# Kernel tuning notes

Measured on AMD Instinct MI355X. Metric: run time of the kernel, lower is better.

## Reference

```python
import jax, jax.numpy as jnp
import numpy as np

B, L, D_MODEL = 2, 2048, 1024
HEADS, DH, K = 8, 128, 64  # d_head = d_model // heads, kernel_width window
DILATIONS = np.array([1, 1, 2, 2, 4, 4, 8, 8], dtype=np.int32)  # per-head dilation


def setup_inputs() -> dict:
    key = jax.random.key(0)
    ks = jax.random.split(key, 8)
    s_in = 1.0 / np.sqrt(D_MODEL)       # kaiming-uniform-ish fan_in bound
    s_c = 1.0 / np.sqrt(HEADS * DH)
    return {
        "query": jax.random.normal(ks[0], (B, L, D_MODEL), dtype=jnp.float32),
        "key": jax.random.normal(ks[1], (B, L, D_MODEL), dtype=jnp.float32),
        "value": jax.random.normal(ks[2], (B, L, D_MODEL), dtype=jnp.float32),
        "Wq": jax.random.uniform(ks[3], (HEADS, DH, D_MODEL), minval=-s_in, maxval=s_in),
        "bq": jnp.zeros((HEADS, DH), dtype=jnp.float32),
        "Wk": jax.random.uniform(ks[4], (HEADS, DH, D_MODEL), minval=-s_in, maxval=s_in),
        "bk": jnp.zeros((HEADS, DH), dtype=jnp.float32),
        "Wv": jax.random.uniform(ks[5], (HEADS, DH, D_MODEL), minval=-s_in, maxval=s_in),
        "bv": jnp.zeros((HEADS, DH), dtype=jnp.float32),
        "Wc": jax.random.uniform(ks[6], (D_MODEL, HEADS * DH), minval=-s_c, maxval=s_c),
        "bc": jnp.zeros((D_MODEL,), dtype=jnp.float32),
    }


def reference(query, key, value, Wq, bq, Wk, bk, Wv, bv, Wc, bc):
    Lq = query.shape[-2]
    # per-head linear projections: [B,L,D] x [H,DH,D] -> [B,H,L,DH]
    q = jnp.einsum('bld,hed->bhle', query, Wq) + bq[:, None, :]
    k = jnp.einsum('bld,hed->bhle', key, Wk) + bk[:, None, :]
    v = jnp.einsum('bld,hed->bhle', value, Wv) + bv[:, None, :]

    # dilated, centered local windows (per-head dilation)
    offsets = jnp.arange(K) - (K - 1) // 2                     # [K]
    dil = jnp.asarray(DILATIONS)                               # [H]
    idx = (jnp.arange(Lq)[None, :, None]
           + offsets[None, None, :] * dil[:, None, None])      # [H, L, K]
    valid = (idx >= 0) & (idx < Lq)
    idxc = jnp.clip(idx, 0, Lq - 1)

    # gather per-head windows: x [B,H,L,DH], idx [H,L,K] -> [B,H,L,K,DH]
    gather = jax.vmap(lambda xh, ih: xh[:, ih], in_axes=(1, 0), out_axes=1)
    k_win = gather(k, idxc)
    v_win = gather(v, idxc)

    # banded attention (original applies no 1/sqrt(d) scaling)
    scores = jnp.einsum('bhld,bhlkd->bhlk', q, k_win)
    scores = jnp.where(valid[None], scores, jnp.asarray(-1e9, scores.dtype))
    attn = jax.nn.softmax(scores, axis=-1)
    out = jnp.einsum('bhlk,bhlkd->bhld', attn, v_win)

    # merge heads and collapse back to d_model
    out = out.transpose(0, 2, 1, 3).reshape(out.shape[0], Lq, HEADS * DH)
    return out @ Wc.T + bc
```

## Files before the change

### kernel.cpp

```cpp
#include <hip/hip_runtime.h>
#include <hip/hip_bf16.h>
#include <stdint.h>

#define NB 2
#define LQ 2048
#define DMODEL 1024
#define NH 8
#define DH 128
#define KWIN 64

typedef __attribute__((ext_vector_type(8))) short short8;
typedef __attribute__((ext_vector_type(4))) float f32x4;

__device__ __forceinline__ ushort f2bf(float f) {
  uint u = __float_as_uint(f);
  return (ushort)((u + 0x7fffu + ((u >> 16) & 1u)) >> 16);
}
__device__ __forceinline__ float bflo(uint u) { return __uint_as_float(u << 16); }
__device__ __forceinline__ float bfhi(uint u) { return __uint_as_float(u & 0xffff0000u); }

__global__ void cvt_all(const float4* __restrict__ q, const float4* __restrict__ k,
                        const float4* __restrict__ v, const float4* __restrict__ wq,
                        const float4* __restrict__ wk, const float4* __restrict__ wv,
                        const float4* __restrict__ wc, ushort4* __restrict__ dst) {
  const int n4in = (NB * LQ * DMODEL) / 4;
  const int n4w = (NH * DH * DMODEL) / 4;
  const int total = 3 * n4in + 4 * n4w;
  const int stride = gridDim.x * blockDim.x;
  for (int i = blockIdx.x * blockDim.x + threadIdx.x; i < total; i += stride) {
    const float4* src;
    int off;
    if (i < 3 * n4in) {
      const int r = i >> 20;
      off = i & (n4in - 1);
      src = (r == 0) ? q : ((r == 1) ? k : v);
    } else {
      const int j = i - 3 * n4in;
      const int r = j >> 18;
      off = j & (n4w - 1);
      src = (r == 0) ? wq : ((r == 1) ? wk : ((r == 2) ? wv : wc));
    }
    float4 x = src[off];
    dst[i] = make_ushort4(f2bf(x.x), f2bf(x.y), f2bf(x.z), f2bf(x.w));
  }
}

__global__ __launch_bounds__(512, 2) void gemm256_qkv(
    const ushort* __restrict__ A0, const ushort* __restrict__ B0,
    const float* __restrict__ c0, ushort* __restrict__ D0,
    const ushort* __restrict__ A1, const ushort* __restrict__ B1,
    const float* __restrict__ c1, ushort* __restrict__ D1,
    const ushort* __restrict__ A2, const ushort* __restrict__ B2,
    const float* __restrict__ c2, ushort* __restrict__ D2,
    int M, int N, int Kd) {
  const int gx = gridDim.x, gy = gridDim.y;
  const int nblk = gx * gy * gridDim.z;
  const int fid = (blockIdx.z * gy + blockIdx.y) * gx + blockIdx.x;
  const int cpx = nblk >> 3;
  const int nid = (fid & 7) * cpx + (fid >> 3);
  const int z = nid / (gx * gy);
  const int rem = nid % (gx * gy);
  const int m0 = (rem / gx) * 256;
  const int n0 = (rem % gx) * 256;

  const ushort* A = (z == 0) ? A0 : ((z == 1) ? A1 : A2);
  const ushort* Bt = (z == 0) ? B0 : ((z == 1) ? B1 : B2);
  const float* bias = (z == 0) ? c0 : ((z == 1) ? c1 : c2);
  ushort* Cv = (z == 0) ? D0 : ((z == 1) ? D1 : D2);

  __shared__ ushort LDS[4 * 16384];

  const int tid = threadIdx.x;
  const int wave = tid >> 6, lane = tid & 63;
  const int wm = wave >> 2, wn = wave & 3;
  const int lrow = lane & 15, kgrp = lane >> 4;

  const int b = tid * 16;
  const int srow = b >> 6;
  const int scc = (b & 63) >> 1;

  const ushort* gA0 = A + (size_t)(m0 + srow) * Kd + scc;
  const ushort* gA1 = A + (size_t)(m0 + 128 + srow) * Kd + scc;
  const ushort* gB0 = Bt + (size_t)(n0 + srow) * Kd + scc;
  const ushort* gB1 = Bt + (size_t)(n0 + 128 + srow) * Kd + scc;
  const int dso = b >> 1;

  auto STAGE = [&](int slot, int kt) {
    ushort* sl = LDS + slot * 16384;
    __builtin_amdgcn_global_load_lds(
        (const __attribute__((address_space(1))) void*)(gA0 + kt),
        (__attribute__((address_space(3))) void*)(sl + dso), 16, 0, 0);
    __builtin_amdgcn_global_load_lds(
        (const __attribute__((address_space(1))) void*)(gA1 + kt),
        (__attribute__((address_space(3))) void*)(sl + 4096 + dso), 16, 0, 0);
    __builtin_amdgcn_global_load_lds(
        (const __attribute__((address_space(1))) void*)(gB0 + kt),
        (__attribute__((address_space(3))) void*)(sl + 8192 + dso), 16, 0, 0);
    __builtin_amdgcn_global_load_lds(
        (const __attribute__((address_space(1))) void*)(gB1 + kt),
        (__attribute__((address_space(3))) void*)(sl + 12288 + dso), 16, 0, 0);
  };

  f32x4 acc[8][4] = {};
  const int NT = Kd >> 5;

  STAGE(0, 0);
  STAGE(1, 32);
  STAGE(2, 64);

  for (int t = 0; t < NT; ++t) {
    const int pf = t + 3;
    if (pf < NT) {
      STAGE(pf & 3, pf << 5);
      asm volatile("s_waitcnt vmcnt(12)" ::: "memory");
    } else if (pf == NT) {
      asm volatile("s_waitcnt vmcnt(8)" ::: "memory");
    } else if (pf == NT + 1) {
      asm volatile("s_waitcnt vmcnt(4)" ::: "memory");
    } else {
      asm volatile("s_waitcnt vmcnt(0)" ::: "memory");
    }
    __builtin_amdgcn_s_barrier();
    __builtin_amdgcn_sched_barrier(0);

    const ushort* sA = LDS + (t & 3) * 16384 + wm * 4096 + lrow * 32 + kgrp * 8;
    const ushort* sB = LDS + (t & 3) * 16384 + 8192 + (wn >> 1) * 4096 +
                       ((wn & 1) * 64 + lrow) * 32 + kgrp * 8;
    short8 af[8], bfr[4];
#pragma unroll
    for (int m = 0; m < 8; ++m) af[m] = *(const short8*)(sA + m * 512);
#pragma unroll
    for (int n = 0; n < 4; ++n) bfr[n] = *(const short8*)(sB + n * 512);
    asm volatile("s_waitcnt lgkmcnt(0)" ::: "memory");
    __builtin_amdgcn_sched_barrier(0);
    __builtin_amdgcn_s_barrier();

#pragma unroll
    for (int m = 0; m < 8; ++m)
#pragma unroll
      for (int n = 0; n < 4; ++n)
        acc[m][n] = __builtin_amdgcn_mfma_f32_16x16x32_bf16(af[m], bfr[n], acc[m][n], 0, 0, 0);
  }

  const int cbase = n0 + wn * 64;
  const int rbase = m0 + wm * 128;
  float bv[4];
#pragma unroll
  for (int n = 0; n < 4; ++n) bv[n] = bias[cbase + n * 16 + lrow];

#pragma unroll
  for (int m = 0; m < 8; ++m) {
#pragma unroll
    for (int n = 0; n < 4; ++n) {
      const int col = cbase + n * 16 + lrow;
#pragma unroll
      for (int j = 0; j < 4; ++j) {
        const int row = rbase + m * 16 + kgrp * 4 + j;
        Cv[(size_t)row * N + col] = f2bf(acc[m][n][j] + bv[n]);
      }
    }
  }
}

__global__ __launch_bounds__(256, 4) void gemm_out(
    const ushort* __restrict__ A, const ushort* __restrict__ Bt,
    const float* __restrict__ bias, float* __restrict__ Cv, int M, int N, int Kd) {
  const int gx = gridDim.x, gy = gridDim.y;
  const int nblk = gx * gy;
  const int fid = blockIdx.y * gx + blockIdx.x;
  const int cpx = nblk >> 3;
  const int nid = (fid & 7) * cpx + (fid >> 3);
  const int m0 = (nid / gx) * 128;
  const int n0 = (nid % gx) * 128;

  __shared__ ushort As[2][128 * 32];
  __shared__ ushort Bs[2][128 * 32];

  const int tid = threadIdx.x;
  const int wave = tid >> 6, lane = tid & 63;
  const int wm = wave >> 1, wn = wave & 1;
  const int lrow = lane & 15, kgrp = lane >> 4;

  const int b0 = tid * 16;
  const int b1 = b0 + 4096;
  const int r0 = b0 >> 6, cc0 = (b0 & 63) >> 1;
  const int r1 = b1 >> 6, cc1 = (b1 & 63) >> 1;

  const ushort* gA0 = A + (size_t)(m0 + r0) * Kd + cc0;
  const ushort* gA1 = A + (size_t)(m0 + r1) * Kd + cc1;
  const ushort* gB0 = Bt + (size_t)(n0 + r0) * Kd + cc0;
  const ushort* gB1 = Bt + (size_t)(n0 + r1) * Kd + cc1;

  auto stage = [&](int buf, int kt) {
    __builtin_amdgcn_global_load_lds(
        (const __attribute__((address_space(1))) void*)(gA0 + kt),
        (__attribute__((address_space(3))) void*)(As[buf] + (b0 >> 1)), 16, 0, 0);
    __builtin_amdgcn_global_load_lds(
        (const __attribute__((address_space(1))) void*)(gA1 + kt),
        (__attribute__((address_space(3))) void*)(As[buf] + (b1 >> 1)), 16, 0, 0);
    __builtin_amdgcn_global_load_lds(
        (const __attribute__((address_space(1))) void*)(gB0 + kt),
        (__attribute__((address_space(3))) void*)(Bs[buf] + (b0 >> 1)), 16, 0, 0);
    __builtin_amdgcn_global_load_lds(
        (const __attribute__((address_space(1))) void*)(gB1 + kt),
        (__attribute__((address_space(3))) void*)(Bs[buf] + (b1 >> 1)), 16, 0, 0);
  };

  f32x4 acc[4][4] = {};

  auto compute = [&](int buf) {
    short8 af[4], bfr[4];
#pragma unroll
    for (int m = 0; m < 4; ++m)
      af[m] = *(const short8*)(As[buf] + (wm * 64 + m * 16 + lrow) * 32 + kgrp * 8);
#pragma unroll
    for (int n = 0; n < 4; ++n)
      bfr[n] = *(const short8*)(Bs[buf] + (wn * 64 + n * 16 + lrow) * 32 + kgrp * 8);
#pragma unroll
    for (int m = 0; m < 4; ++m)
#pragma unroll
      for (int n = 0; n < 4; ++n)
        acc[m][n] = __builtin_amdgcn_mfma_f32_16x16x32_bf16(af[m], bfr[n], acc[m][n], 0, 0, 0);
  };

  const int nt = Kd >> 5;
  stage(0, 0);
  __syncthreads();
  int cur = 0;
  for (int it = 0; it < nt - 1; ++it) {
    stage(cur ^ 1, (it + 1) << 5);
    compute(cur);
    __syncthreads();
    cur ^= 1;
  }
  compute(cur);

  const int cbase = n0 + wn * 64;
  const int rbase = m0 + wm * 64;
  float bv[4];
#pragma unroll
  for (int n = 0; n < 4; ++n) bv[n] = bias[cbase + n * 16 + lrow];

#pragma unroll
  for (int m = 0; m < 4; ++m) {
#pragma unroll
    for (int n = 0; n < 4; ++n) {
      const int col = cbase + n * 16 + lrow;
#pragma unroll
      for (int j = 0; j < 4; ++j) {
        const int row = rbase + m * 16 + kgrp * 4 + j;
        Cv[(size_t)row * N + col] = acc[m][n][j] + bv[n];
      }
    }
  }
}

__global__ __launch_bounds__(128) void banded_attn_mfma(
    const ushort* __restrict__ qp, const ushort* __restrict__ kp,
    const ushort* __restrict__ vp, ushort* __restrict__ ao) {
  __shared__ ushort Qs[32 * 128];
  __shared__ ushort Ks[96 * 128];
  __shared__ ushort Vs[112 * 128];
  __shared__ ushort Ps[2][16 * 104];
  __shared__ ushort Os[2][16 * 128];

  const int tid = threadIdx.x;
  const int wv = tid >> 6;
  const int lane = tid & 63;
  const int lrow = lane & 15, kgrp = lane >> 4;

  const int blk = blockIdx.x;
  const int chunk = blk & 63;
  const int h = (blk >> 6) & 7;
  const int b = blk >> 9;
  const int sh = h >> 1;
  const int dil = 1 << sh;
  const int Ld = LQ >> sh;
  const int rres = chunk >> (6 - sh);
  const int tile = chunk & ((64 >> sh) - 1);
  const int t0 = tile << 5;
  const int p0 = t0 - 32;

  const size_t headoff = (size_t)h * DH;
  const size_t bbase = (size_t)b * LQ * (NH * DH);

  const int srow = lane >> 4;
  const int sc = lane & 15;
  for (int it = wv; it < 60; it += 2) {
    int rbase, pstart;
    const ushort* g;
    ushort* ld;
    if (it < 8) {
      rbase = it * 4; pstart = t0; g = qp; ld = Qs;
    } else if (it < 32) {
      rbase = (it - 8) * 4; pstart = p0; g = kp; ld = Ks;
    } else {
      rbase = (it - 32) * 4; pstart = p0; g = vp; ld = Vs;
    }
    int row = rbase + srow;
    int key = (row ^ (row >> 3)) & 7;
    int cs = sc ^ key;
    int t = pstart + row;
    t = t < 0 ? 0 : (t >= Ld ? Ld - 1 : t);
    int l = rres + t * dil;
    const ushort* src = g + bbase + (size_t)l * (NH * DH) + headoff + cs * 8;
    __builtin_amdgcn_global_load_lds(
        (const __attribute__((address_space(1))) void*)src,
        (__attribute__((address_space(3))) void*)(ld + rbase * 128), 16, 0, 0);
  }
  __syncthreads();

  const int iblk = wv << 4;
  f32x4 accs[5] = {};
#pragma unroll
  for (int ks = 0; ks < 4; ++ks) {
    const int qrow = iblk + lrow;
    const int qslot = (ks * 4 + kgrp) ^ ((qrow ^ (qrow >> 3)) & 7);
    short8 qf = *(const short8*)(Qs + qrow * 128 + qslot * 8);
#pragma unroll
    for (int t = 0; t < 5; ++t) {
      const int krow = (wv + t) * 16 + lrow;
      const int kslot = (ks * 4 + kgrp) ^ ((krow ^ (krow >> 3)) & 7);
      short8 kf = *(const short8*)(Ks + krow * 128 + kslot * 8);
      accs[t] = __builtin_amdgcn_mfma_f32_16x16x32_bf16(qf, kf, accs[t], 0, 0, 0);
    }
  }

  float dens[4];
#pragma unroll
  for (int j = 0; j < 4; ++j) {
    const int i_b = iblk + kgrp * 4 + j;
    float mj = -1e30f;
#pragma unroll
    for (int t = 0; t < 5; ++t) {
      const int jj = (wv + t) * 16 + lrow;
      const int p = p0 + jj;
      const bool ok = (jj >= i_b + 1) && (jj <= i_b + 64) && (p >= 0) && (p < Ld);
      float v = ok ? accs[t][j] : -1e30f;
      accs[t][j] = v;
      mj = fmaxf(mj, v);
    }
#pragma unroll
    for (int off = 1; off < 16; off <<= 1) mj = fmaxf(mj, __shfl_xor(mj, off));
    float dj = 0.f;
#pragma unroll
    for (int t = 0; t < 5; ++t) {
      float e = __expf(accs[t][j] - mj);
      accs[t][j] = e;
      dj += e;
    }
#pragma unroll
    for (int off = 1; off < 16; off <<= 1) dj += __shfl_xor(dj, off);
    dens[j] = dj;
  }

  ushort* Pw = Ps[wv];
#pragma unroll
  for (int j = 0; j < 4; ++j) {
    const int prow = kgrp * 4 + j;
#pragma unroll
    for (int t = 0; t < 5; ++t) Pw[prow * 104 + t * 16 + lrow] = f2bf(accs[t][j]);
    Pw[prow * 104 + 80 + lrow] = 0;
  }

  f32x4 accv[8] = {};
#pragma unroll
  for (int ks = 0; ks < 3; ++ks) {
    short8 pf = *(const short8*)(Pw + lrow * 104 + ks * 32 + kgrp * 8);
#pragma unroll
    for (int dt = 0; dt < 8; ++dt) {
      short8 vf;
#pragma unroll
      for (int rr = 0; rr < 8; ++rr) {
        const int vrow = iblk + ks * 32 + kgrp * 8 + rr;
        const int d = dt * 16 + lrow;
        const int slot = (d >> 3) ^ ((vrow ^ (vrow >> 3)) & 7);
        vf[rr] = (short)Vs[vrow * 128 + slot * 8 + (d & 7)];
      }
      accv[dt] = __builtin_amdgcn_mfma_f32_16x16x32_bf16(pf, vf, accv[dt], 0, 0, 0);
    }
  }

  ushort* Ow = Os[wv];
#pragma unroll
  for (int j = 0; j < 4; ++j) {
    const float inv = 1.f / dens[j];
    const int orow = kgrp * 4 + j;
#pragma unroll
    for (int dt = 0; dt < 8; ++dt)
      Ow[orow * 128 + dt * 16 + lrow] = f2bf(accv[dt][j] * inv);
  }
#pragma unroll
  for (int pass = 0; pass < 4; ++pass) {
    const int i_loc = pass * 4 + srow;
    const int tq = t0 + iblk + i_loc;
    const int l = rres + tq * dil;
    short8 vvv = *(const short8*)(Ow + i_loc * 128 + sc * 8);
    *(short8*)(ao + bbase + (size_t)l * (NH * DH) + headoff + sc * 8) = vvv;
  }
}

extern "C" void kernel_launch(void* const* d_in, const int* in_sizes, int n_in,
                              void* d_out, int out_size, void* d_ws, size_t ws_size,
                              hipStream_t stream) {
  const float* q = (const float*)d_in[0];
  const float* k = (const float*)d_in[1];
  const float* v = (const float*)d_in[2];
  const float* Wq = (const float*)d_in[3];
  const float* bq = (const float*)d_in[4];
  const float* Wk = (const float*)d_in[5];
  const float* bk = (const float*)d_in[6];
  const float* Wv = (const float*)d_in[7];
  const float* bv = (const float*)d_in[8];
  const float* Wc = (const float*)d_in[9];
  const float* bc = (const float*)d_in[10];

  const size_t NIN = (size_t)NB * LQ * DMODEL;
  const size_t NW = (size_t)NH * DH * DMODEL;

  ushort* qin = (ushort*)d_ws;
  ushort* kin = qin + NIN;
  ushort* vin = kin + NIN;
  ushort* wqb = vin + NIN;
  ushort* wkb = wqb + NW;
  ushort* wvb = wkb + NW;
  ushort* wcb = wvb + NW;
  ushort* qp = wcb + NW;
  ushort* kp = qp + NIN;
  ushort* vp = kp + NIN;
  ushort* aob = vp + NIN;

  hipLaunchKernelGGL(cvt_all, dim3(2048), dim3(256), 0, stream,
                     (const float4*)q, (const float4*)k, (const float4*)v,
                     (const float4*)Wq, (const float4*)Wk, (const float4*)Wv,
                     (const float4*)Wc, (ushort4*)qin);

  dim3 g1(DMODEL / 256, (NB * LQ) / 256, 3);
  hipLaunchKernelGGL(gemm256_qkv, g1, dim3(512), 0, stream,
                     qin, wqb, bq, qp,
                     kin, wkb, bk, kp,
                     vin, wvb, bv, vp,
                     NB * LQ, DMODEL, DMODEL);

  hipLaunchKernelGGL(banded_attn_mfma, dim3(NB * NH * 64), dim3(128), 0, stream,
                     qp, kp, vp, aob);

  dim3 g2(DMODEL / 128, (NB * LQ) / 128);
  hipLaunchKernelGGL(gemm_out, g2, dim3(256), 0, stream,
                     aob, wcb, bc, (float*)d_out, NB * LQ, DMODEL, DMODEL);
}
```

Measured before the change: 104.0 us.

## Swizzle QKV GEMM LDS layout and split stage loads across MFMA halves

The QKV projection GEMM gets an XOR-swizzled LDS layout that pairs rows, meant to reduce bank conflicts on the fragment reads. Each k-step is now split into two MFMA halves, with the next tile's global-to-LDS loads issued half before and half between them. Prefetch depth drops from three to two tiles and the second barrier is removed. The MFMA blocks are also wrapped in s_setprio. This adds scheduling complexity and carries a risk of LDS races now that a barrier is gone and the pipeline is shallower.

Result: faster. 99.81 us (-4.0%).

```diff
diff --git a/kernel.cpp b/kernel.cpp
--- a/kernel.cpp
+++ b/kernel.cpp
@@ -11,6 +11,9 @@
 
 typedef __attribute__((ext_vector_type(8))) short short8;
 typedef __attribute__((ext_vector_type(4))) float f32x4;
+
+#define AS1 __attribute__((address_space(1)))
+#define AS3 __attribute__((address_space(3)))
 
 __device__ __forceinline__ ushort f2bf(float f) {
   uint u = __float_as_uint(f);
@@ -45,7 +48,7 @@
   }
 }
 
-__global__ __launch_bounds__(512, 2) void gemm256_qkv(
+__global__ __launch_bounds__(512, 2) void gemm256p(
     const ushort* __restrict__ A0, const ushort* __restrict__ B0,
     const float* __restrict__ c0, ushort* __restrict__ D0,
     const ushort* __restrict__ A1, const ushort* __restrict__ B1,
@@ -68,78 +71,99 @@
   const float* bias = (z == 0) ? c0 : ((z == 1) ? c1 : c2);
   ushort* Cv = (z == 0) ? D0 : ((z == 1) ? D1 : D2);
 
-  __shared__ ushort LDS[4 * 16384];
+  __shared__ ushort LDS[4][16384];
 
   const int tid = threadIdx.x;
   const int wave = tid >> 6, lane = tid & 63;
   const int wm = wave >> 2, wn = wave & 3;
   const int lrow = lane & 15, kgrp = lane >> 4;
 
-  const int b = tid * 16;
-  const int srow = b >> 6;
-  const int scc = (b & 63) >> 1;
-
-  const ushort* gA0 = A + (size_t)(m0 + srow) * Kd + scc;
-  const ushort* gA1 = A + (size_t)(m0 + 128 + srow) * Kd + scc;
-  const ushort* gB0 = Bt + (size_t)(n0 + srow) * Kd + scc;
-  const ushort* gB1 = Bt + (size_t)(n0 + 128 + srow) * Kd + scc;
-  const int dso = b >> 1;
-
-  auto STAGE = [&](int slot, int kt) {
-    ushort* sl = LDS + slot * 16384;
-    __builtin_amdgcn_global_load_lds(
-        (const __attribute__((address_space(1))) void*)(gA0 + kt),
-        (__attribute__((address_space(3))) void*)(sl + dso), 16, 0, 0);
-    __builtin_amdgcn_global_load_lds(
-        (const __attribute__((address_space(1))) void*)(gA1 + kt),
-        (__attribute__((address_space(3))) void*)(sl + 4096 + dso), 16, 0, 0);
-    __builtin_amdgcn_global_load_lds(
-        (const __attribute__((address_space(1))) void*)(gB0 + kt),
-        (__attribute__((address_space(3))) void*)(sl + 8192 + dso), 16, 0, 0);
-    __builtin_amdgcn_global_load_lds(
-        (const __attribute__((address_space(1))) void*)(gB1 + kt),
-        (__attribute__((address_space(3))) void*)(sl + 12288 + dso), 16, 0, 0);
+  const ushort* gsrc[4];
+  int lofs[4];
+#pragma unroll
+  for (int qq = 0; qq < 4; ++qq) {
+    const int half = qq & 1;
+    const int o = half * 8192 + tid * 16;
+    const int pr = o >> 7;
+    const int s = (o >> 4) & 7;
+    const int x = s ^ (pr & 7);
+    const int row = 2 * pr + (x & 1);
+    const int chunk = (x >> 1) * 8;
+    lofs[qq] = (qq >> 1) * 8192 + half * 4096 + tid * 8;
+    gsrc[qq] = (qq < 2) ? (A + (size_t)(m0 + row) * Kd + chunk)
+                        : (Bt + (size_t)(n0 + row) * Kd + chunk);
+  }
+
+  auto STAGE2 = [&](int tt, int p) {
+    ushort* sl = &LDS[tt & 3][0];
+    const int kt = tt << 5;
+    __builtin_amdgcn_global_load_lds((const AS1 void*)(gsrc[p] + kt),
+                                     (AS3 void*)(sl + lofs[p]), 16, 0, 0);
+    __builtin_amdgcn_global_load_lds((const AS1 void*)(gsrc[2 + p] + kt),
+                                     (AS3 void*)(sl + lofs[2 + p]), 16, 0, 0);
   };
+
+  int aoff[8], boff[4];
+#pragma unroll
+  for (int mi = 0; mi < 8; ++mi) {
+    const int r = wm * 128 + mi * 16 + lrow;
+    aoff[mi] = (r >> 1) * 64 + ((((kgrp << 1) | (r & 1)) ^ ((r >> 1) & 7)) * 8);
+  }
+#pragma unroll
+  for (int ni = 0; ni < 4; ++ni) {
+    const int r = wn * 64 + ni * 16 + lrow;
+    boff[ni] = 8192 + (r >> 1) * 64 + ((((kgrp << 1) | (r & 1)) ^ ((r >> 1) & 7)) * 8);
+  }
 
   f32x4 acc[8][4] = {};
   const int NT = Kd >> 5;
 
-  STAGE(0, 0);
-  STAGE(1, 32);
-  STAGE(2, 64);
+  STAGE2(0, 0); STAGE2(0, 1);
+  STAGE2(1, 0); STAGE2(1, 1);
 
   for (int t = 0; t < NT; ++t) {
-    const int pf = t + 3;
-    if (pf < NT) {
-      STAGE(pf & 3, pf << 5);
-      asm volatile("s_waitcnt vmcnt(12)" ::: "memory");
-    } else if (pf == NT) {
-      asm volatile("s_waitcnt vmcnt(8)" ::: "memory");
-    } else if (pf == NT + 1) {
+    const ushort* sl = &LDS[t & 3][0];
+    if (t < NT - 2) {
+      STAGE2(t + 2, 0);
+      asm volatile("s_waitcnt vmcnt(6)" ::: "memory");
+    } else if (t == NT - 2) {
       asm volatile("s_waitcnt vmcnt(4)" ::: "memory");
     } else {
       asm volatile("s_waitcnt vmcnt(0)" ::: "memory");
     }
+    __builtin_amdgcn_sched_barrier(0);
     __builtin_amdgcn_s_barrier();
     __builtin_amdgcn_sched_barrier(0);
 
-    const ushort* sA = LDS + (t & 3) * 16384 + wm * 4096 + lrow * 32 + kgrp * 8;
-    const ushort* sB = LDS + (t & 3) * 16384 + 8192 + (wn >> 1) * 4096 +
-                       ((wn & 1) * 64 + lrow) * 32 + kgrp * 8;
     short8 af[8], bfr[4];
 #pragma unroll
-    for (int m = 0; m < 8; ++m) af[m] = *(const short8*)(sA + m * 512);
-#pragma unroll
-    for (int n = 0; n < 4; ++n) bfr[n] = *(const short8*)(sB + n * 512);
+    for (int m = 0; m < 4; ++m) af[m] = *(const short8*)(sl + aoff[m]);
+#pragma unroll
+    for (int n = 0; n < 4; ++n) bfr[n] = *(const short8*)(sl + boff[n]);
     asm volatile("s_waitcnt lgkmcnt(0)" ::: "memory");
     __builtin_amdgcn_sched_barrier(0);
-    __builtin_amdgcn_s_barrier();
-
-#pragma unroll
-    for (int m = 0; m < 8; ++m)
+    __builtin_amdgcn_s_setprio(1);
+#pragma unroll
+    for (int m = 0; m < 4; ++m)
 #pragma unroll
       for (int n = 0; n < 4; ++n)
         acc[m][n] = __builtin_amdgcn_mfma_f32_16x16x32_bf16(af[m], bfr[n], acc[m][n], 0, 0, 0);
+    __builtin_amdgcn_s_setprio(0);
+    __builtin_amdgcn_sched_barrier(0);
+
+    if (t < NT - 2) STAGE2(t + 2, 1);
+#pragma unroll
+    for (int m = 4; m < 8; ++m) af[m] = *(const short8*)(sl + aoff[m]);
+    asm volatile("s_waitcnt lgkmcnt(0)" ::: "memory");
+    __builtin_amdgcn_sched_barrier(0);
+    __builtin_amdgcn_s_setprio(1);
+#pragma unroll
+    for (int m = 4; m < 8; ++m)
+#pragma unroll
+      for (int n = 0; n < 4; ++n)
+        acc[m][n] = __builtin_amdgcn_mfma_f32_16x16x32_bf16(af[m], bfr[n], acc[m][n], 0, 0, 0);
+    __builtin_amdgcn_s_setprio(0);
+    __builtin_amdgcn_sched_barrier(0);
   }
 
   const int cbase = n0 + wn * 64;
@@ -192,18 +216,14 @@
   const ushort* gB1 = Bt + (size_t)(n0 + r1) * Kd + cc1;
 
   auto stage = [&](int buf, int kt) {
-    __builtin_amdgcn_global_load_lds(
-        (const __attribute__((address_space(1))) void*)(gA0 + kt),
-        (__attribute__((address_space(3))) void*)(As[buf] + (b0 >> 1)), 16, 0, 0);
-    __builtin_amdgcn_global_load_lds(
-        (const __attribute__((address_space(1))) void*)(gA1 + kt),
-        (__attribute__((address_space(3))) void*)(As[buf] + (b1 >> 1)), 16, 0, 0);
-    __builtin_amdgcn_global_load_lds(
-        (const __attribute__((address_space(1))) void*)(gB0 + kt),
-        (__attribute__((address_space(3))) void*)(Bs[buf] + (b0 >> 1)), 16, 0, 0);
-    __builtin_amdgcn_global_load_lds(
-        (const __attribute__((address_space(1))) void*)(gB1 + kt),
-        (__attribute__((address_space(3))) void*)(Bs[buf] + (b1 >> 1)), 16, 0, 0);
+    __builtin_amdgcn_global_load_lds((const AS1 void*)(gA0 + kt),
+                                     (AS3 void*)(As[buf] + (b0 >> 1)), 16, 0, 0);
+    __builtin_amdgcn_global_load_lds((const AS1 void*)(gA1 + kt),
+                                     (AS3 void*)(As[buf] + (b1 >> 1)), 16, 0, 0);
+    __builtin_amdgcn_global_load_lds((const AS1 void*)(gB0 + kt),
+                                     (AS3 void*)(Bs[buf] + (b0 >> 1)), 16, 0, 0);
+    __builtin_amdgcn_global_load_lds((const AS1 void*)(gB1 + kt),
+                                     (AS3 void*)(Bs[buf] + (b1 >> 1)), 16, 0, 0);
   };
 
   f32x4 acc[4][4] = {};
@@ -304,9 +324,8 @@
     t = t < 0 ? 0 : (t >= Ld ? Ld - 1 : t);
     int l = rres + t * dil;
     const ushort* src = g + bbase + (size_t)l * (NH * DH) + headoff + cs * 8;
-    __builtin_amdgcn_global_load_lds(
-        (const __attribute__((address_space(1))) void*)src,
-        (__attribute__((address_space(3))) void*)(ld + rbase * 128), 16, 0, 0);
+    __builtin_amdgcn_global_load_lds((const AS1 void*)src,
+                                     (AS3 void*)(ld + rbase * 128), 16, 0, 0);
   }
   __syncthreads();
 
@@ -436,7 +455,7 @@
                      (const float4*)Wc, (ushort4*)qin);
 
   dim3 g1(DMODEL / 256, (NB * LQ) / 256, 3);
-  hipLaunchKernelGGL(gemm256_qkv, g1, dim3(512), 0, stream,
+  hipLaunchKernelGGL(gemm256p, g1, dim3(512), 0, stream,
                      qin, wqb, bq, qp,
                      kin, wkb, bk, kp,
                      vin, wvb, bv, vp,
```
